# Performance work log

Hardware: AMD Instinct MI355X
Metric: run time of the kernel (lower is better)

## Reference

```python
import jax, jax.numpy as jnp
import numpy as np

# Forest of B perfect binary trees, depth D levels, M = 2**D - 1 nodes/tree.
B, D, H, X, VOCAB, NCLS = 32, 12, 256, 256, 32000, 20
M = 2 ** D - 1          # 4095 nodes per tree
N = B * M               # 131040 total nodes


def setup_inputs() -> dict:
    key = jax.random.key(0)
    ks = jax.random.split(key, 9)
    x = jax.random.randint(ks[0], (N,), 0, VOCAB, dtype=jnp.int32)
    # leaves are the last level of each tree: in-tree index >= 2**(D-1)-1
    leaf = (jnp.arange(M) >= 2 ** (D - 1) - 1).astype(jnp.int32)
    x_mask = jnp.tile(leaf, B)  # [N] int32, 1 on leaves, 0 on internal nodes
    s = 0.02
    Emb = jax.random.normal(ks[1], (VOCAB, X), jnp.float32) * s
    W_iou = jax.random.normal(ks[2], (3 * H, X), jnp.float32) * s
    b_iou = jnp.zeros((3 * H,), jnp.float32)
    U_iou = jax.random.normal(ks[3], (3 * H, H), jnp.float32) * s
    U_f = jax.random.normal(ks[4], (H, H), jnp.float32) * s
    b_f = jnp.ones((H,), jnp.float32)  # forget-gate bias init
    W_out = jax.random.normal(ks[5], (NCLS, H), jnp.float32) * s
    b_out = jnp.zeros((NCLS,), jnp.float32)
    return {"x": x, "x_mask": x_mask, "Emb": Emb, "W_iou": W_iou,
            "b_iou": b_iou, "U_iou": U_iou, "U_f": U_f, "b_f": b_f,
            "W_out": W_out, "b_out": b_out}


def reference(x, x_mask, Emb, W_iou, b_iou, U_iou, U_f, b_f, W_out, b_out):
    # input_module: embedding applied to masked ids, result masked again
    x_emb = Emb[x * x_mask] * x_mask[:, None].astype(Emb.dtype)      # [N, X]
    xiou = (x_emb @ W_iou.T).reshape(B, M, 3 * H)                    # W_iou * x per node
    h_sum = jnp.zeros((B, M, H), Emb.dtype)    # sum of children h (childsum)
    fc_sum = jnp.zeros((B, M, H), Emb.dtype)   # sum_k f_k * c_k from children
    h_all = jnp.zeros((B, M, H), Emb.dtype)
    # topological propagation: leaves (deepest level) -> roots
    for l in range(D - 1, -1, -1):
        s_, e_ = 2 ** l - 1, 2 ** (l + 1) - 1  # static in-tree level slice
        iou = xiou[:, s_:e_] + h_sum[:, s_:e_] @ U_iou.T + b_iou
        i, o, u = jnp.split(iou, 3, axis=-1)
        c = jax.nn.sigmoid(i) * jnp.tanh(u) + fc_sum[:, s_:e_]
        h = jax.nn.sigmoid(o) * jnp.tanh(c)
        h_all = h_all.at[:, s_:e_].set(h)
        if l > 0:
            f = jax.nn.sigmoid(h @ U_f.T + b_f)          # per-child forget gate
            parents = (np.arange(s_, e_) - 1) // 2       # static parent indices
            h_sum = h_sum.at[:, parents].add(h)
            fc_sum = fc_sum.at[:, parents].add(f * c)
    # output_module applied to all node states
    return h_all.reshape(N, H) @ W_out.T + b_out                    # [N, NCLS]
```

## Files before the change

### kernel.cpp

```cpp
#include <hip/hip_runtime.h>

#define B_TREES 32
#define DEPTH   12
#define M_NODES 4095
#define N_NODES (B_TREES * M_NODES)
#define HDIM    256
#define VOCAB   32000
#define NCLS    20
#define LEAFROWS 65536
#define LDSH_S 20

typedef _Float16 f16;
typedef _Float16 f16x8 __attribute__((ext_vector_type(8)));
typedef _Float16 f16x4 __attribute__((ext_vector_type(4)));
typedef _Float16 f16x2 __attribute__((ext_vector_type(2)));
typedef float    f32x4 __attribute__((ext_vector_type(4)));

__device__ __forceinline__ float sigf(float x)      { return 1.0f / (1.0f + __expf(-x)); }
__device__ __forceinline__ float tanh_fast(float x) { return 1.0f - 2.0f / (1.0f + __expf(2.0f * x)); }

__global__ __launch_bounds__(256) void cvt_kernel(
    const float4* __restrict__ Emb,  const float4* __restrict__ Wiou,
    const float4* __restrict__ Uiou, const float4* __restrict__ Uf,
    const float4* __restrict__ Wout,
    f16x4* __restrict__ Emb16,  f16x4* __restrict__ Wiou16,
    f16x4* __restrict__ Uiou16, f16x4* __restrict__ Uf16,
    f16x4* __restrict__ Wout16)
{
    int i = blockIdx.x * 256 + threadIdx.x;
    if (i < VOCAB * HDIM / 4) {
        float4 v = Emb[i];
        f16x4 r; r[0] = (f16)v.x; r[1] = (f16)v.y; r[2] = (f16)v.z; r[3] = (f16)v.w;
        Emb16[i] = r;
    }
    if (i < 768 * HDIM / 4) {
        float4 v = Wiou[i];
        f16x4 r; r[0] = (f16)v.x; r[1] = (f16)v.y; r[2] = (f16)v.z; r[3] = (f16)v.w;
        Wiou16[i] = r;
        float4 u = Uiou[i];
        f16x4 s; s[0] = (f16)u.x; s[1] = (f16)u.y; s[2] = (f16)u.z; s[3] = (f16)u.w;
        Uiou16[i] = s;
    }
    if (i < HDIM * HDIM / 4) {
        float4 v = Uf[i];
        f16x4 r; r[0] = (f16)v.x; r[1] = (f16)v.y; r[2] = (f16)v.z; r[3] = (f16)v.w;
        Uf16[i] = r;
    }
    if (i < 32 * HDIM / 4) {
        int row = i >> 6;
        f16x4 r = {};
        if (row < NCLS) {
            float4 v = Wout[i];
            r[0] = (f16)v.x; r[1] = (f16)v.y; r[2] = (f16)v.z; r[3] = (f16)v.w;
        }
        Wout16[i] = r;
    }
}

#define VTPW 5
__global__ __launch_bounds__(256) void vocab_kernel(
    const f16* __restrict__ Emb16, const f16* __restrict__ Wiou16,
    const float* __restrict__ b_iou,
    f16* __restrict__ hv, f16* __restrict__ cv)
{
    __shared__ f16 wlds[1536 * 8];
    __shared__ f16 ldshH[4][16 * LDSH_S];
    __shared__ f16 ldshC[4][16 * LDSH_S];

    const int tid  = threadIdx.x;
    const int lane = tid & 63;
    const int w    = tid >> 6;
    const int quad = lane >> 4;
    const int l15  = lane & 15;
    const int qk   = quad * 8;
    const int cb0  = blockIdx.x * 16;

    #pragma unroll
    for (int i = 0; i < 6; ++i) {
        int f = i * 256 + tid;
        int mat = f >> 9, r = f & 511, ks = r >> 6, q = (r >> 4) & 3, c = r & 15;
        *(f16x8*)(wlds + f * 8) = *(const f16x8*)(Wiou16 +
            (mat * 256 + cb0 + c) * HDIM + ks * 32 + q * 8);
    }
    __syncthreads();

    const float bi = b_iou[cb0 + l15];
    const float bo = b_iou[256 + cb0 + l15];
    const float bu = b_iou[512 + cb0 + l15];

    const int row0 = (blockIdx.y * 4 + w) * (VTPW * 16);

    f16x8 a[8];
    #pragma unroll
    for (int ks = 0; ks < 8; ++ks)
        a[ks] = *(const f16x8*)(Emb16 + (row0 + l15) * HDIM + ks * 32 + qk);

    for (int rt = 0; rt < VTPW; ++rt) {
        const int rw = row0 + rt * 16;
        f16x8 ac[8];
        #pragma unroll
        for (int ks = 0; ks < 8; ++ks) ac[ks] = a[ks];

        if (rt + 1 < VTPW) {
            #pragma unroll
            for (int ks = 0; ks < 8; ++ks)
                a[ks] = *(const f16x8*)(Emb16 + (rw + 16 + l15) * HDIM + ks * 32 + qk);
        }

        f32x4 acc[3] = {};
        #pragma unroll
        for (int ks = 0; ks < 8; ++ks) {
            #pragma unroll
            for (int mat = 0; mat < 3; ++mat) {
                f16x8 wf = *(const f16x8*)(wlds +
                    ((mat * 8 + ks) * 64 + quad * 16 + l15) * 8);
                acc[mat] = __builtin_amdgcn_mfma_f32_16x16x32_f16(
                    ac[ks], wf, acc[mat], 0, 0, 0);
            }
        }

        #pragma unroll
        for (int r = 0; r < 4; ++r) {
            float i_ = acc[0][r] + bi;
            float o_ = acc[1][r] + bo;
            float u_ = acc[2][r] + bu;
            float c  = sigf(i_) * tanh_fast(u_);
            float h  = sigf(o_) * tanh_fast(c);
            ldshH[w][(quad * 4 + r) * LDSH_S + l15] = (f16)h;
            ldshC[w][(quad * 4 + r) * LDSH_S + l15] = (f16)c;
        }

        {
            int row_l = lane >> 2, cpos = (lane & 3) * 4;
            f16x4 vh = *(const f16x4*)(&ldshH[w][row_l * LDSH_S + cpos]);
            *(f16x4*)(hv + (rw + row_l) * HDIM + cb0 + cpos) = vh;
            f16x4 vc = *(const f16x4*)(&ldshC[w][row_l * LDSH_S + cpos]);
            *(f16x4*)(cv + (rw + row_l) * HDIM + cb0 + cpos) = vc;
        }
    }
}

__global__ __launch_bounds__(256) void vocab_out_kernel(
    const f16* __restrict__ hv, const f16* __restrict__ Wout16,
    const float* __restrict__ bout, float* __restrict__ out_v)
{
    const int lane = threadIdx.x & 63;
    const int w    = threadIdx.x >> 6;
    const int quad = lane >> 4;
    const int l15  = lane & 15;
    const int qk   = quad * 8;

    f16x8 wfk[2][8];
    #pragma unroll
    for (int cf = 0; cf < 2; ++cf)
        #pragma unroll
        for (int ks = 0; ks < 8; ++ks)
            wfk[cf][ks] = *(const f16x8*)(Wout16 +
                (cf * 16 + l15) * HDIM + ks * 32 + qk);
    float bo[2];
    #pragma unroll
    for (int cf = 0; cf < 2; ++cf) {
        int col = cf * 16 + l15;
        bo[cf] = bout[col < NCLS ? col : 0];
    }

    const int tile0 = blockIdx.x * 16;

    for (int rt = w; rt < 16; rt += 4) {
        const int rw = (tile0 + rt) * 16;
        f32x4 acc[2] = {};
        #pragma unroll
        for (int ks = 0; ks < 8; ++ks) {
            f16x8 a = *(const f16x8*)(hv + (rw + l15) * HDIM + ks * 32 + qk);
            #pragma unroll
            for (int cf = 0; cf < 2; ++cf)
                acc[cf] = __builtin_amdgcn_mfma_f32_16x16x32_f16(
                    a, wfk[cf][ks], acc[cf], 0, 0, 0);
        }
        #pragma unroll
        for (int cf = 0; cf < 2; ++cf) {
            const int col = cf * 16 + l15;
            if (col < NCLS) {
                #pragma unroll
                for (int r = 0; r < 4; ++r)
                    out_v[(rw + quad * 4 + r) * NCLS + col] = acc[cf][r] + bo[cf];
            }
        }
    }
}

__global__ __launch_bounds__(256) void leaf_scatter_kernel(
    const int* __restrict__ x, const f16* __restrict__ hv,
    const f16* __restrict__ cv, const float* __restrict__ out_v,
    f16* __restrict__ h16, f16* __restrict__ cT, float* __restrict__ out)
{
    __shared__ int ids[64];
    __shared__ f16 ldsc[64][HDIM + 8];

    const int tid = threadIdx.x;
    const int R0  = blockIdx.x * 64;

    if (tid < 64) {
        int r = R0 + tid;
        int node = (r >> 11) * M_NODES + 2047 + (r & 2047);
        ids[tid] = x[node];
    }
    __syncthreads();

    const int r    = tid >> 2;
    const int p    = tid & 3;
    const int id   = ids[r];
    const int gr   = R0 + r;
    const int node = (gr >> 11) * M_NODES + 2047 + (gr & 2047);

    #pragma unroll
    for (int j = 0; j < 8; ++j) {
        f16x8 v = *(const f16x8*)(hv + id * HDIM + p * 64 + j * 8);
        *(f16x8*)(h16 + node * HDIM + p * 64 + j * 8) = v;
    }
    #pragma unroll
    for (int j = 0; j < 8; ++j) {
        f16x8 v = *(const f16x8*)(cv + id * HDIM + p * 64 + j * 8);
        *(f16x8*)(&ldsc[r][p * 64 + j * 8]) = v;
    }
    #pragma unroll
    for (int j = 0; j < 5; ++j)
        out[node * NCLS + p * 5 + j] = out_v[id * NCLS + p * 5 + j];

    __syncthreads();

    {
        const int c = tid;
        f16 tmp[64];
        #pragma unroll
        for (int rr = 0; rr < 64; ++rr) tmp[rr] = ldsc[rr][c];
        #pragma unroll
        for (int j = 0; j < 8; ++j)
            *(f16x8*)(cT + c * LEAFROWS + R0 + j * 8) = *(const f16x8*)(&tmp[j * 8]);
    }
}

__global__ __launch_bounds__(512) void fused_level_kernel(
    const f16* __restrict__ Uiou16, const f16* __restrict__ Uf16,
    const float* __restrict__ b_iou, const float* __restrict__ b_f,
    f16* __restrict__ h16, const f16* __restrict__ cT_child,
    f16* __restrict__ cT_parent, int l, int rows_p)
{
    __shared__ f16 wlds[2048 * 8];
    __shared__ f16 ldsh[8][16 * LDSH_S];

    const int tid  = threadIdx.x;
    const int lane = tid & 63;
    const int w    = tid >> 6;
    const int quad = lane >> 4;
    const int l15  = lane & 15;
    const int qk   = quad * 8;
    const int cb0  = blockIdx.x * 16;

    #pragma unroll
    for (int i = 0; i < 4; ++i) {
        int f = i * 512 + tid;
        int mat = f >> 9, r = f & 511, ks = r >> 6, q = (r >> 4) & 3, c = r & 15;
        const f16* src = (mat == 0)
            ? (Uf16 + (cb0 + c) * HDIM + ks * 32 + q * 8)
            : (Uiou16 + ((mat - 1) * 256 + cb0 + c) * HDIM + ks * 32 + q * 8);
        *(f16x8*)(wlds + f * 8) = *(const f16x8*)src;
    }
    __syncthreads();

    const int pw = blockIdx.y * 128 + w * 16;
    if (pw >= rows_p) return;

    const float bi  = b_iou[cb0 + l15];
    const float bo  = b_iou[256 + cb0 + l15];
    const float bu  = b_iou[512 + cb0 + l15];
    const float bfv = b_f[cb0 + l15];
    const int lc = l + 1;
    const int maskc = (1 << lc) - 1;
    const int maskp = (1 << l) - 1;
    const int rows_c = rows_p * 2;
    const int cw = 2 * pw;

    int childBase0, childBase1;
    {
        int cl0 = cw + l15;
        childBase0 = ((cl0 >> lc) * M_NODES + maskc + (cl0 & maskc)) * HDIM;
        int cl1 = cw + 16 + l15;
        childBase1 = ((cl1 >> lc) * M_NODES + maskc + (cl1 & maskc)) * HDIM;
    }

    f32x4 accf0 = {}, accf1 = {};
    f32x4 au0[3] = {}, au1[3] = {};
    #pragma unroll
    for (int ks = 0; ks < 8; ++ks) {
        const int k0 = ks * 32 + qk;
        f16x8 a0 = *(const f16x8*)(h16 + childBase0 + k0);
        f16x8 a1 = *(const f16x8*)(h16 + childBase1 + k0);
        f16x8 wfF = *(const f16x8*)(wlds + (ks * 64 + quad * 16 + l15) * 8);
        accf0 = __builtin_amdgcn_mfma_f32_16x16x32_f16(a0, wfF, accf0, 0, 0, 0);
        accf1 = __builtin_amdgcn_mfma_f32_16x16x32_f16(a1, wfF, accf1, 0, 0, 0);
        #pragma unroll
        for (int m = 0; m < 3; ++m) {
            f16x8 wm = *(const f16x8*)(wlds +
                (((m + 1) * 8 + ks) * 64 + quad * 16 + l15) * 8);
            au0[m] = __builtin_amdgcn_mfma_f32_16x16x32_f16(a0, wm, au0[m], 0, 0, 0);
            au1[m] = __builtin_amdgcn_mfma_f32_16x16x32_f16(a1, wm, au1[m], 0, 0, 0);
        }
    }

    #pragma unroll
    for (int s = 0; s < 2; ++s) {
        const f32x4& af = s ? accf1 : accf0;
        const f32x4* au = s ? au1 : au0;
        const int csr = cw + s * 16;
        f16x4 cc = *(const f16x4*)(cT_child +
            (cb0 + l15) * rows_c + csr + quad * 4);
        f16x2 cpack;
        #pragma unroll
        for (int pr = 0; pr < 2; ++pr) {
            float f0 = sigf(af[2 * pr]     + bfv);
            float f1 = sigf(af[2 * pr + 1] + bfv);
            float fc = f0 * (float)cc[2 * pr] + f1 * (float)cc[2 * pr + 1];
            float i_ = au[0][2 * pr] + au[0][2 * pr + 1] + bi;
            float o_ = au[1][2 * pr] + au[1][2 * pr + 1] + bo;
            float u_ = au[2][2 * pr] + au[2][2 * pr + 1] + bu;
            float c  = sigf(i_) * tanh_fast(u_) + fc;
            float h  = sigf(o_) * tanh_fast(c);
            cpack[pr] = (f16)c;
            ldsh[w][(s * 8 + quad * 2 + pr) * LDSH_S + l15] = (f16)h;
        }
        *(f16x2*)(cT_parent + (cb0 + l15) * rows_p + pw + s * 8 + quad * 2) = cpack;
    }

    {
        int prow = lane >> 2, cpos = (lane & 3) * 4;
        int p = pw + prow;
        int b = p >> l, tt = p & maskp;
        int node = b * M_NODES + (1 << l) - 1 + tt;
        f16x4 v = *(const f16x4*)(&ldsh[w][prow * LDSH_S + cpos]);
        *(f16x4*)(h16 + node * HDIM + cb0 + cpos) = v;
    }
}

__global__ __launch_bounds__(256) void out_kernel(
    const f16* __restrict__ h16, const f16* __restrict__ Wout16,
    const float* __restrict__ bout, float* __restrict__ out)
{
    const int lane = threadIdx.x & 63;
    const int w    = threadIdx.x >> 6;
    const int quad = lane >> 4;
    const int l15  = lane & 15;
    const int qk   = quad * 8;

    f16x8 wfk[2][8];
    #pragma unroll
    for (int cf = 0; cf < 2; ++cf)
        #pragma unroll
        for (int ks = 0; ks < 8; ++ks)
            wfk[cf][ks] = *(const f16x8*)(Wout16 +
                (cf * 16 + l15) * HDIM + ks * 32 + qk);
    float bo[2];
    #pragma unroll
    for (int cf = 0; cf < 2; ++cf) {
        int col = cf * 16 + l15;
        bo[cf] = bout[col < NCLS ? col : 0];
    }

    const int tile0 = blockIdx.x * 16;

    for (int rt = w; rt < 16; rt += 4) {
        const int tt = tile0 + rt;
        const int rw = (tt >> 7) * M_NODES + (tt & 127) * 16;
        f32x4 acc[2] = {};
        #pragma unroll
        for (int ks = 0; ks < 8; ++ks) {
            f16x8 a = *(const f16x8*)(h16 + (rw + l15) * HDIM + ks * 32 + qk);
            #pragma unroll
            for (int cf = 0; cf < 2; ++cf)
                acc[cf] = __builtin_amdgcn_mfma_f32_16x16x32_f16(
                    a, wfk[cf][ks], acc[cf], 0, 0, 0);
        }
        #pragma unroll
        for (int cf = 0; cf < 2; ++cf) {
            const int col = cf * 16 + l15;
            if (col < NCLS) {
                #pragma unroll
                for (int r = 0; r < 4; ++r)
                    out[(rw + quad * 4 + r) * NCLS + col] = acc[cf][r] + bo[cf];
            }
        }
    }
}

extern "C" void kernel_launch(void* const* d_in, const int* in_sizes, int n_in,
                              void* d_out, int out_size, void* d_ws, size_t ws_size,
                              hipStream_t stream)
{
    const int*   x     = (const int*)d_in[0];
    const float* Emb   = (const float*)d_in[2];
    const float* W_iou = (const float*)d_in[3];
    const float* b_iou = (const float*)d_in[4];
    const float* U_iou = (const float*)d_in[5];
    const float* U_f   = (const float*)d_in[6];
    const float* b_f   = (const float*)d_in[7];
    const float* W_out = (const float*)d_in[8];
    const float* b_out = (const float*)d_in[9];
    float* out = (float*)d_out;

    char* ws = (char*)d_ws;
    size_t off = 0;
    auto take = [&](size_t bytes) -> char* {
        char* p = ws + off; off += (bytes + 255) & ~(size_t)255; return p;
    };
    f16* h16    = (f16*)take((size_t)N_NODES * HDIM * 2);
    f16* cA     = (f16*)take((size_t)HDIM * LEAFROWS * 2);
    f16* cB     = (f16*)take((size_t)HDIM * (LEAFROWS / 2) * 2);
    f16* Emb16  = (f16*)take((size_t)VOCAB * HDIM * 2);
    f16* Wiou16 = (f16*)take((size_t)768 * HDIM * 2);
    f16* Uiou16 = (f16*)take((size_t)768 * HDIM * 2);
    f16* Uf16   = (f16*)take((size_t)HDIM * HDIM * 2);
    f16* Wout16 = (f16*)take((size_t)32 * HDIM * 2);
    f16* cv     = (f16*)take((size_t)VOCAB * HDIM * 2);
    float* outv = (float*)take((size_t)VOCAB * NCLS * 4);
    f16* hv     = cB;

    cvt_kernel<<<VOCAB * HDIM / 4 / 256, 256, 0, stream>>>(
        (const float4*)Emb, (const float4*)W_iou, (const float4*)U_iou,
        (const float4*)U_f, (const float4*)W_out,
        (f16x4*)Emb16, (f16x4*)Wiou16, (f16x4*)Uiou16, (f16x4*)Uf16,
        (f16x4*)Wout16);

    vocab_kernel<<<dim3(16, VOCAB / (4 * 16 * VTPW)), 256, 0, stream>>>(
        Emb16, Wiou16, b_iou, hv, cv);

    vocab_out_kernel<<<dim3(VOCAB / 16 / 16), 256, 0, stream>>>(
        hv, Wout16, b_out, outv);

    leaf_scatter_kernel<<<dim3(LEAFROWS / 64), 256, 0, stream>>>(
        x, hv, cv, outv, h16, cA, out);

    f16* cin  = cA;
    f16* cout_ = cB;
    for (int l = 10; l >= 0; --l) {
        int rows_p = B_TREES << l;
        int gy = (rows_p + 127) / 128;
        fused_level_kernel<<<dim3(16, gy), 512, 0, stream>>>(
            Uiou16, Uf16, b_iou, b_f, h16, cin, cout_, l, rows_p);
        f16* t = cin; cin = cout_; cout_ = t;
    }

    out_kernel<<<dim3(32 * 128 / 16), 256, 0, stream>>>(
        h16, Wout16, b_out, out);
}
```

Before: 425.7 us.

## Swizzle block IDs across XCDs and prefetch child rows before MFMA loop

Flattens the vocab and level kernel grids to 1D and remaps block IDs so that blocks on the same XCD handle the same row stripe across column groups. The intent is for child h rows and embedding rows to be reused in each XCD's private L2. The level kernel also loads all child h fragments and child c values into registers before the MFMA loop, which exposes more memory parallelism. It adds a launch-bounds occupancy hint of 4 blocks per CU. The costs are higher register pressure, and some vocab blocks are launched only to exit early.

```diff
diff --git a/kernel.cpp b/kernel.cpp
--- a/kernel.cpp
+++ b/kernel.cpp
@@ -67,13 +67,20 @@
     __shared__ f16 ldshH[4][16 * LDSH_S];
     __shared__ f16 ldshC[4][16 * LDSH_S];
 
+    const int id     = blockIdx.x;
+    const int xcd    = id & 7;
+    const int slot   = id >> 3;
+    const int cg     = slot & 15;
+    const int stripe = xcd * 13 + (slot >> 4);
+    if (stripe >= 100) return;
+
     const int tid  = threadIdx.x;
     const int lane = tid & 63;
     const int w    = tid >> 6;
     const int quad = lane >> 4;
     const int l15  = lane & 15;
     const int qk   = quad * 8;
-    const int cb0  = blockIdx.x * 16;
+    const int cb0  = cg * 16;
 
     #pragma unroll
     for (int i = 0; i < 6; ++i) {
@@ -88,7 +95,7 @@
     const float bo = b_iou[256 + cb0 + l15];
     const float bu = b_iou[512 + cb0 + l15];
 
-    const int row0 = (blockIdx.y * 4 + w) * (VTPW * 16);
+    const int row0 = (stripe * 4 + w) * (VTPW * 16);
 
     f16x8 a[8];
     #pragma unroll
@@ -240,14 +247,24 @@
     }
 }
 
-__global__ __launch_bounds__(512) void fused_level_kernel(
+__global__ __launch_bounds__(512, 4) void fused_level_kernel(
     const f16* __restrict__ Uiou16, const f16* __restrict__ Uf16,
     const float* __restrict__ b_iou, const float* __restrict__ b_f,
     f16* __restrict__ h16, const f16* __restrict__ cT_child,
-    f16* __restrict__ cT_parent, int l, int rows_p)
+    f16* __restrict__ cT_parent, int l, int rows_p, int nstripes, int swz)
 {
     __shared__ f16 wlds[2048 * 8];
     __shared__ f16 ldsh[8][16 * LDSH_S];
+
+    const int id = blockIdx.x;
+    int stripe, cg;
+    if (swz) {
+        cg     = (id >> 3) & 15;
+        stripe = (id & 7) * (nstripes >> 3) + (id >> 7);
+    } else {
+        cg     = id & 15;
+        stripe = id >> 4;
+    }
 
     const int tid  = threadIdx.x;
     const int lane = tid & 63;
@@ -255,7 +272,7 @@
     const int quad = lane >> 4;
     const int l15  = lane & 15;
     const int qk   = quad * 8;
-    const int cb0  = blockIdx.x * 16;
+    const int cb0  = cg * 16;
 
     #pragma unroll
     for (int i = 0; i < 4; ++i) {
@@ -268,7 +285,7 @@
     }
     __syncthreads();
 
-    const int pw = blockIdx.y * 128 + w * 16;
+    const int pw = stripe * 128 + w * 16;
     if (pw >= rows_p) return;
 
     const float bi  = b_iou[cb0 + l15];
@@ -289,22 +306,29 @@
         childBase1 = ((cl1 >> lc) * M_NODES + maskc + (cl1 & maskc)) * HDIM;
     }
 
+    f16x8 a0[8], a1[8];
+    #pragma unroll
+    for (int ks = 0; ks < 8; ++ks) {
+        const int k0 = ks * 32 + qk;
+        a0[ks] = *(const f16x8*)(h16 + childBase0 + k0);
+        a1[ks] = *(const f16x8*)(h16 + childBase1 + k0);
+    }
+    f16x4 cc0 = *(const f16x4*)(cT_child + (cb0 + l15) * rows_c + cw + quad * 4);
+    f16x4 cc1 = *(const f16x4*)(cT_child + (cb0 + l15) * rows_c + cw + 16 + quad * 4);
+
     f32x4 accf0 = {}, accf1 = {};
     f32x4 au0[3] = {}, au1[3] = {};
     #pragma unroll
     for (int ks = 0; ks < 8; ++ks) {
-        const int k0 = ks * 32 + qk;
-        f16x8 a0 = *(const f16x8*)(h16 + childBase0 + k0);
-        f16x8 a1 = *(const f16x8*)(h16 + childBase1 + k0);
         f16x8 wfF = *(const f16x8*)(wlds + (ks * 64 + quad * 16 + l15) * 8);
-        accf0 = __builtin_amdgcn_mfma_f32_16x16x32_f16(a0, wfF, accf0, 0, 0, 0);
-        accf1 = __builtin_amdgcn_mfma_f32_16x16x32_f16(a1, wfF, accf1, 0, 0, 0);
+        accf0 = __builtin_amdgcn_mfma_f32_16x16x32_f16(a0[ks], wfF, accf0, 0, 0, 0);
+        accf1 = __builtin_amdgcn_mfma_f32_16x16x32_f16(a1[ks], wfF, accf1, 0, 0, 0);
         #pragma unroll
         for (int m = 0; m < 3; ++m) {
             f16x8 wm = *(const f16x8*)(wlds +
                 (((m + 1) * 8 + ks) * 64 + quad * 16 + l15) * 8);
-            au0[m] = __builtin_amdgcn_mfma_f32_16x16x32_f16(a0, wm, au0[m], 0, 0, 0);
-            au1[m] = __builtin_amdgcn_mfma_f32_16x16x32_f16(a1, wm, au1[m], 0, 0, 0);
+            au0[m] = __builtin_amdgcn_mfma_f32_16x16x32_f16(a0[ks], wm, au0[m], 0, 0, 0);
+            au1[m] = __builtin_amdgcn_mfma_f32_16x16x32_f16(a1[ks], wm, au1[m], 0, 0, 0);
         }
     }
 
@@ -312,9 +336,7 @@
     for (int s = 0; s < 2; ++s) {
         const f32x4& af = s ? accf1 : accf0;
         const f32x4* au = s ? au1 : au0;
-        const int csr = cw + s * 16;
-        f16x4 cc = *(const f16x4*)(cT_child +
-            (cb0 + l15) * rows_c + csr + quad * 4);
+        f16x4 cc = s ? cc1 : cc0;
         f16x2 cpack;
         #pragma unroll
         for (int pr = 0; pr < 2; ++pr) {
@@ -430,7 +452,7 @@
         (f16x4*)Emb16, (f16x4*)Wiou16, (f16x4*)Uiou16, (f16x4*)Uf16,
         (f16x4*)Wout16);
 
-    vocab_kernel<<<dim3(16, VOCAB / (4 * 16 * VTPW)), 256, 0, stream>>>(
+    vocab_kernel<<<8 * 13 * 16, 256, 0, stream>>>(
         Emb16, Wiou16, b_iou, hv, cv);
 
     vocab_out_kernel<<<dim3(VOCAB / 16 / 16), 256, 0, stream>>>(
@@ -443,9 +465,10 @@
     f16* cout_ = cB;
     for (int l = 10; l >= 0; --l) {
         int rows_p = B_TREES << l;
-        int gy = (rows_p + 127) / 128;
-        fused_level_kernel<<<dim3(16, gy), 512, 0, stream>>>(
-            Uiou16, Uf16, b_iou, b_f, h16, cin, cout_, l, rows_p);
+        int nstripes = (rows_p + 127) / 128;
+        int swz = (nstripes % 8 == 0) ? 1 : 0;
+        fused_level_kernel<<<nstripes * 16, 512, 0, stream>>>(
+            Uiou16, Uf16, b_iou, b_f, h16, cin, cout_, l, rows_p, nstripes, swz);
         f16* t = cin; cin = cout_; cout_ = t;
     }
 
```

Result: no change. 424.3 us (-0.3%).

## Remap blocks to XCD-aware stripes and loop over stripes in large levels

Applied to the files above, without the earlier changes.

The vocab kernel and the fused level kernel now use a 1D grid. Block IDs are remapped so that blocks sharing row stripes land on the same XCD (id&7), which is meant to improve L2 locality of the child h rows across the 16 column-group blocks. For the large levels (l>=8), a fixed 512-block persistent grid loops over stripes, so the LDS weight load is paid once per block instead of once per stripe. In exchange, the vocab grid wastes a few blocks (stripe>=100 exits early) and the looped levels get less parallelism per launch.

```diff
diff --git a/kernel.cpp b/kernel.cpp
--- a/kernel.cpp
+++ b/kernel.cpp
@@ -67,13 +67,20 @@
     __shared__ f16 ldshH[4][16 * LDSH_S];
     __shared__ f16 ldshC[4][16 * LDSH_S];
 
+    const int id     = blockIdx.x;
+    const int xcd    = id & 7;
+    const int slot   = id >> 3;
+    const int cg     = slot & 15;
+    const int stripe = xcd * 13 + (slot >> 4);
+    if (stripe >= 100) return;
+
     const int tid  = threadIdx.x;
     const int lane = tid & 63;
     const int w    = tid >> 6;
     const int quad = lane >> 4;
     const int l15  = lane & 15;
     const int qk   = quad * 8;
-    const int cb0  = blockIdx.x * 16;
+    const int cb0  = cg * 16;
 
     #pragma unroll
     for (int i = 0; i < 6; ++i) {
@@ -88,7 +95,7 @@
     const float bo = b_iou[256 + cb0 + l15];
     const float bu = b_iou[512 + cb0 + l15];
 
-    const int row0 = (blockIdx.y * 4 + w) * (VTPW * 16);
+    const int row0 = (stripe * 4 + w) * (VTPW * 16);
 
     f16x8 a[8];
     #pragma unroll
@@ -244,10 +251,27 @@
     const f16* __restrict__ Uiou16, const f16* __restrict__ Uf16,
     const float* __restrict__ b_iou, const float* __restrict__ b_f,
     f16* __restrict__ h16, const f16* __restrict__ cT_child,
-    f16* __restrict__ cT_parent, int l, int rows_p)
+    f16* __restrict__ cT_parent, int l, int rows_p, int nstripes, int looped)
 {
     __shared__ f16 wlds[2048 * 8];
     __shared__ f16 ldsh[8][16 * LDSH_S];
+
+    const int id = blockIdx.x;
+    int cg, sbase, sfirst, scount, sstep;
+    if (looped) {
+        cg     = (id >> 3) & 15;
+        int spx = nstripes >> 3;
+        sbase  = (id & 7) * spx;
+        sfirst = id >> 7;
+        scount = spx;
+        sstep  = 4;
+    } else {
+        cg     = id & 15;
+        sbase  = id >> 4;
+        sfirst = 0;
+        scount = 1;
+        sstep  = 1;
+    }
 
     const int tid  = threadIdx.x;
     const int lane = tid & 63;
@@ -255,7 +279,7 @@
     const int quad = lane >> 4;
     const int l15  = lane & 15;
     const int qk   = quad * 8;
-    const int cb0  = blockIdx.x * 16;
+    const int cb0  = cg * 16;
 
     #pragma unroll
     for (int i = 0; i < 4; ++i) {
@@ -267,9 +291,6 @@
         *(f16x8*)(wlds + f * 8) = *(const f16x8*)src;
     }
     __syncthreads();
-
-    const int pw = blockIdx.y * 128 + w * 16;
-    if (pw >= rows_p) return;
 
     const float bi  = b_iou[cb0 + l15];
     const float bo  = b_iou[256 + cb0 + l15];
@@ -279,66 +300,72 @@
     const int maskc = (1 << lc) - 1;
     const int maskp = (1 << l) - 1;
     const int rows_c = rows_p * 2;
-    const int cw = 2 * pw;
-
-    int childBase0, childBase1;
-    {
-        int cl0 = cw + l15;
-        childBase0 = ((cl0 >> lc) * M_NODES + maskc + (cl0 & maskc)) * HDIM;
-        int cl1 = cw + 16 + l15;
-        childBase1 = ((cl1 >> lc) * M_NODES + maskc + (cl1 & maskc)) * HDIM;
-    }
-
-    f32x4 accf0 = {}, accf1 = {};
-    f32x4 au0[3] = {}, au1[3] = {};
-    #pragma unroll
-    for (int ks = 0; ks < 8; ++ks) {
-        const int k0 = ks * 32 + qk;
-        f16x8 a0 = *(const f16x8*)(h16 + childBase0 + k0);
-        f16x8 a1 = *(const f16x8*)(h16 + childBase1 + k0);
-        f16x8 wfF = *(const f16x8*)(wlds + (ks * 64 + quad * 16 + l15) * 8);
-        accf0 = __builtin_amdgcn_mfma_f32_16x16x32_f16(a0, wfF, accf0, 0, 0, 0);
-        accf1 = __builtin_amdgcn_mfma_f32_16x16x32_f16(a1, wfF, accf1, 0, 0, 0);
-        #pragma unroll
-        for (int m = 0; m < 3; ++m) {
-            f16x8 wm = *(const f16x8*)(wlds +
-                (((m + 1) * 8 + ks) * 64 + quad * 16 + l15) * 8);
-            au0[m] = __builtin_amdgcn_mfma_f32_16x16x32_f16(a0, wm, au0[m], 0, 0, 0);
-            au1[m] = __builtin_amdgcn_mfma_f32_16x16x32_f16(a1, wm, au1[m], 0, 0, 0);
-        }
-    }
-
-    #pragma unroll
-    for (int s = 0; s < 2; ++s) {
-        const f32x4& af = s ? accf1 : accf0;
-        const f32x4* au = s ? au1 : au0;
-        const int csr = cw + s * 16;
-        f16x4 cc = *(const f16x4*)(cT_child +
-            (cb0 + l15) * rows_c + csr + quad * 4);
-        f16x2 cpack;
-        #pragma unroll
-        for (int pr = 0; pr < 2; ++pr) {
-            float f0 = sigf(af[2 * pr]     + bfv);
-            float f1 = sigf(af[2 * pr + 1] + bfv);
-            float fc = f0 * (float)cc[2 * pr] + f1 * (float)cc[2 * pr + 1];
-            float i_ = au[0][2 * pr] + au[0][2 * pr + 1] + bi;
-            float o_ = au[1][2 * pr] + au[1][2 * pr + 1] + bo;
-            float u_ = au[2][2 * pr] + au[2][2 * pr + 1] + bu;
-            float c  = sigf(i_) * tanh_fast(u_) + fc;
-            float h  = sigf(o_) * tanh_fast(c);
-            cpack[pr] = (f16)c;
-            ldsh[w][(s * 8 + quad * 2 + pr) * LDSH_S + l15] = (f16)h;
-        }
-        *(f16x2*)(cT_parent + (cb0 + l15) * rows_p + pw + s * 8 + quad * 2) = cpack;
-    }
-
-    {
-        int prow = lane >> 2, cpos = (lane & 3) * 4;
-        int p = pw + prow;
-        int b = p >> l, tt = p & maskp;
-        int node = b * M_NODES + (1 << l) - 1 + tt;
-        f16x4 v = *(const f16x4*)(&ldsh[w][prow * LDSH_S + cpos]);
-        *(f16x4*)(h16 + node * HDIM + cb0 + cpos) = v;
+
+    for (int s = sfirst; s < scount; s += sstep) {
+        const int stripe = sbase + s;
+        const int pw = stripe * 128 + w * 16;
+        if (pw >= rows_p) continue;
+        const int cw = 2 * pw;
+
+        int childBase0, childBase1;
+        {
+            int cl0 = cw + l15;
+            childBase0 = ((cl0 >> lc) * M_NODES + maskc + (cl0 & maskc)) * HDIM;
+            int cl1 = cw + 16 + l15;
+            childBase1 = ((cl1 >> lc) * M_NODES + maskc + (cl1 & maskc)) * HDIM;
+        }
+
+        f32x4 accf0 = {}, accf1 = {};
+        f32x4 au0[3] = {}, au1[3] = {};
+        #pragma unroll
+        for (int ks = 0; ks < 8; ++ks) {
+            const int k0 = ks * 32 + qk;
+            f16x8 a0 = *(const f16x8*)(h16 + childBase0 + k0);
+            f16x8 a1 = *(const f16x8*)(h16 + childBase1 + k0);
+            f16x8 wfF = *(const f16x8*)(wlds + (ks * 64 + quad * 16 + l15) * 8);
+            accf0 = __builtin_amdgcn_mfma_f32_16x16x32_f16(a0, wfF, accf0, 0, 0, 0);
+            accf1 = __builtin_amdgcn_mfma_f32_16x16x32_f16(a1, wfF, accf1, 0, 0, 0);
+            #pragma unroll
+            for (int m = 0; m < 3; ++m) {
+                f16x8 wm = *(const f16x8*)(wlds +
+                    (((m + 1) * 8 + ks) * 64 + quad * 16 + l15) * 8);
+                au0[m] = __builtin_amdgcn_mfma_f32_16x16x32_f16(a0, wm, au0[m], 0, 0, 0);
+                au1[m] = __builtin_amdgcn_mfma_f32_16x16x32_f16(a1, wm, au1[m], 0, 0, 0);
+            }
+        }
+
+        #pragma unroll
+        for (int sh = 0; sh < 2; ++sh) {
+            const f32x4& af = sh ? accf1 : accf0;
+            const f32x4* au = sh ? au1 : au0;
+            const int csr = cw + sh * 16;
+            f16x4 cc = *(const f16x4*)(cT_child +
+                (cb0 + l15) * rows_c + csr + quad * 4);
+            f16x2 cpack;
+            #pragma unroll
+            for (int pr = 0; pr < 2; ++pr) {
+                float f0 = sigf(af[2 * pr]     + bfv);
+                float f1 = sigf(af[2 * pr + 1] + bfv);
+                float fc = f0 * (float)cc[2 * pr] + f1 * (float)cc[2 * pr + 1];
+                float i_ = au[0][2 * pr] + au[0][2 * pr + 1] + bi;
+                float o_ = au[1][2 * pr] + au[1][2 * pr + 1] + bo;
+                float u_ = au[2][2 * pr] + au[2][2 * pr + 1] + bu;
+                float c  = sigf(i_) * tanh_fast(u_) + fc;
+                float h  = sigf(o_) * tanh_fast(c);
+                cpack[pr] = (f16)c;
+                ldsh[w][(sh * 8 + quad * 2 + pr) * LDSH_S + l15] = (f16)h;
+            }
+            *(f16x2*)(cT_parent + (cb0 + l15) * rows_p + pw + sh * 8 + quad * 2) = cpack;
+        }
+
+        {
+            int prow = lane >> 2, cpos = (lane & 3) * 4;
+            int p = pw + prow;
+            int b = p >> l, tt = p & maskp;
+            int node = b * M_NODES + (1 << l) - 1 + tt;
+            f16x4 v = *(const f16x4*)(&ldsh[w][prow * LDSH_S + cpos]);
+            *(f16x4*)(h16 + node * HDIM + cb0 + cpos) = v;
+        }
     }
 }
 
@@ -430,7 +457,7 @@
         (f16x4*)Emb16, (f16x4*)Wiou16, (f16x4*)Uiou16, (f16x4*)Uf16,
         (f16x4*)Wout16);
 
-    vocab_kernel<<<dim3(16, VOCAB / (4 * 16 * VTPW)), 256, 0, stream>>>(
+    vocab_kernel<<<8 * 13 * 16, 256, 0, stream>>>(
         Emb16, Wiou16, b_iou, hv, cv);
 
     vocab_out_kernel<<<dim3(VOCAB / 16 / 16), 256, 0, stream>>>(
@@ -443,9 +470,11 @@
     f16* cout_ = cB;
     for (int l = 10; l >= 0; --l) {
         int rows_p = B_TREES << l;
-        int gy = (rows_p + 127) / 128;
-        fused_level_kernel<<<dim3(16, gy), 512, 0, stream>>>(
-            Uiou16, Uf16, b_iou, b_f, h16, cin, cout_, l, rows_p);
+        int nstripes = (rows_p + 127) / 128;
+        int looped = (l >= 8) ? 1 : 0;
+        int grid = looped ? 512 : nstripes * 16;
+        fused_level_kernel<<<grid, 512, 0, stream>>>(
+            Uiou16, Uf16, b_iou, b_f, h16, cin, cout_, l, rows_p, nstripes, looped);
         f16* t = cin; cin = cout_; cout_ = t;
     }
 
```

New measurement: 396.3 us, median of 3. 6.9% less time.
